# Optimization experiments

Measured on AMD Instinct MI355X. Metric: run time of the kernel, lower is better.

## Reference

```python
import jax, jax.numpy as jnp
import numpy as np

N_NODES = 100000
N_EDGES = 1600000
D_IN = 64
D_HID = 64


def setup_inputs() -> dict:
    key = jax.random.key(0)
    k1, k2, k3, k4, k5 = jax.random.split(key, 5)
    features = jax.random.normal(k1, (N_NODES, D_IN), dtype=jnp.float32)
    src = jax.random.randint(k2, (N_EDGES,), 0, N_NODES, dtype=jnp.int64)
    dst = jax.random.randint(k3, (N_EDGES,), 0, N_NODES, dtype=jnp.int64)
    # nn.Linear(in_feats, n_hidden): W is [out, in], b is [out]
    W = jax.random.normal(k4, (D_HID, D_IN), dtype=jnp.float32) * (1.0 / np.sqrt(D_IN))
    b = jax.random.normal(k5, (D_HID,), dtype=jnp.float32) * 0.01
    return {"features": features, "src": src, "dst": dst, "W": W, "b": b}


def reference(features, src, dst, W, b):
    # copy_src + sum: h_agg[v] = sum_{(u->v) in E} features[u]
    msgs = features[src]                                   # [E, D_IN] gather
    h_agg = jax.ops.segment_sum(msgs, dst, num_segments=N_NODES)  # [N, D_IN] scatter-add
    # NodeApplyModule: linear + activation
    h = h_agg @ W.T + b                                    # [N, D_HID]
    return jax.nn.relu(h)
```

## Files before the change

kernel.cpp:

```cpp
#include <hip/hip_runtime.h>
#include <hip/hip_bf16.h>

constexpr int N_NODES = 100000;
constexpr int N_EDGES = 1600000;
constexpr int D = 64;
constexpr int NPB = 64;
constexpr int NBUK = (N_NODES + NPB - 1) / NPB;
constexpr int CAP = 1536;
constexpr int CAP_E = 2304;
constexpr unsigned SENT = 100000u;
constexpr int PART_BLOCKS = 256;
constexpr int CONV_BLOCKS = 64;
constexpr int PREP_THREADS = 1024;
constexpr int EPB = (N_EDGES + PART_BLOCKS - 1) / PART_BLOCKS;

__device__ inline unsigned pack_bf16_2(float a, float b) {
    unsigned ua = __float_as_uint(a), ub = __float_as_uint(b);
    ua = (ua + 0x7FFFu + ((ua >> 16) & 1u)) >> 16;
    ub = (ub + 0x7FFFu + ((ub >> 16) & 1u)) >> 16;
    return ua | (ub << 16);
}

__global__ __launch_bounds__(PREP_THREADS) void prep_kernel(
    const float* __restrict__ feat, const int* __restrict__ src,
    const int* __restrict__ dst, int* __restrict__ gtot,
    unsigned* __restrict__ packed, uint2* __restrict__ fb) {
    const int tid = threadIdx.x;

    if (blockIdx.x >= PART_BLOCKS) {
        const int cb = blockIdx.x - PART_BLOCKS;
        const int total = N_NODES * D / 4;
        const float4* f4 = reinterpret_cast<const float4*>(feat);
        for (int i = cb * PREP_THREADS + tid; i < total; i += CONV_BLOCKS * PREP_THREADS) {
            const float4 v = f4[i];
            fb[i] = make_uint2(pack_bf16_2(v.x, v.y), pack_bf16_2(v.z, v.w));
        }
        if (cb == 0 && tid < 16)
            fb[(size_t)SENT * 16 + tid] = make_uint2(0u, 0u);
        return;
    }

    __shared__ int lcnt[NBUK];
    __shared__ int lbase[NBUK];

    const int lo = blockIdx.x * EPB;
    int hi = lo + EPB; if (hi > N_EDGES) hi = N_EDGES;

    for (int i = tid; i < NBUK; i += PREP_THREADS) lcnt[i] = 0;
    __syncthreads();

    #pragma unroll 4
    for (int e = lo + tid; e < hi; e += PREP_THREADS)
        atomicAdd(&lcnt[dst[e] >> 6], 1);
    __syncthreads();

    for (int i = tid; i < NBUK; i += PREP_THREADS) {
        const int c = lcnt[i];
        lbase[i] = c ? atomicAdd(&gtot[i], c) : 0;
        lcnt[i] = 0;
    }
    __syncthreads();

    #pragma unroll 4
    for (int e = lo + tid; e < hi; e += PREP_THREADS) {
        const int d = dst[e];
        const int buk = d >> 6;
        const int p = lbase[buk] + atomicAdd(&lcnt[buk], 1);
        if (p < CAP)
            packed[(size_t)buk * CAP + p] =
                ((unsigned)(d & (NPB - 1)) << 17) | (unsigned)src[e];
    }
}

__global__ __launch_bounds__(256, 2) void bucket_kernel(
    const uint2* __restrict__ fb, const int* __restrict__ gtot,
    const unsigned* __restrict__ packed, const float* __restrict__ W,
    const float* __restrict__ bias, float* __restrict__ out) {
    __shared__ unsigned elist[CAP_E];
    __shared__ int cnt[NPB];
    __shared__ int cur[NPB];
    __shared__ int pstart[NPB];
    __shared__ float hrow[4][D];

    const int tid = threadIdx.x;
    const int w = tid >> 6;
    const int j = tid & 63;
    const int g = j >> 4;
    const int l = j & 15;
    const int buk = blockIdx.x;

    float4 wr[16];
    #pragma unroll
    for (int q = 0; q < 16; ++q)
        wr[q] = *reinterpret_cast<const float4*>(W + j * D + (q << 2));
    const float bj = bias[j];

    int m = gtot[buk]; if (m > CAP) m = CAP;
    const unsigned* bp = packed + (size_t)buk * CAP;

    unsigned pk0 = 0, pk1 = 0, pk2 = 0, pk3 = 0, pk4 = 0, pk5 = 0;
    const bool v0 = tid < m,            v1 = tid + 256 < m;
    const bool v2 = tid + 512 < m,      v3 = tid + 768 < m;
    const bool v4 = tid + 1024 < m,     v5 = tid + 1280 < m;
    if (v0) pk0 = bp[tid];
    if (v1) pk1 = bp[tid + 256];
    if (v2) pk2 = bp[tid + 512];
    if (v3) pk3 = bp[tid + 768];
    if (v4) pk4 = bp[tid + 1024];
    if (v5) pk5 = bp[tid + 1280];

    if (tid < NPB) cnt[tid] = 0;
    for (int i = tid; i < CAP_E; i += 256) elist[i] = SENT;
    __syncthreads();

    if (v0) atomicAdd(&cnt[pk0 >> 17], 1);
    if (v1) atomicAdd(&cnt[pk1 >> 17], 1);
    if (v2) atomicAdd(&cnt[pk2 >> 17], 1);
    if (v3) atomicAdd(&cnt[pk3 >> 17], 1);
    if (v4) atomicAdd(&cnt[pk4 >> 17], 1);
    if (v5) atomicAdd(&cnt[pk5 >> 17], 1);
    __syncthreads();

    if (tid < 64) {
        const int c = cnt[tid];
        const int pc = (c + 15) & ~15;
        int x = pc;
        #pragma unroll
        for (int o = 1; o < 64; o <<= 1) {
            const int y = __shfl_up(x, o);
            if (tid >= o) x += y;
        }
        pstart[tid] = x - pc;
        cur[tid] = x - pc;
    }
    __syncthreads();

    if (v0) { const int p = atomicAdd(&cur[pk0 >> 17], 1); elist[p] = pk0 & 0x1FFFFu; }
    if (v1) { const int p = atomicAdd(&cur[pk1 >> 17], 1); elist[p] = pk1 & 0x1FFFFu; }
    if (v2) { const int p = atomicAdd(&cur[pk2 >> 17], 1); elist[p] = pk2 & 0x1FFFFu; }
    if (v3) { const int p = atomicAdd(&cur[pk3 >> 17], 1); elist[p] = pk3 & 0x1FFFFu; }
    if (v4) { const int p = atomicAdd(&cur[pk4 >> 17], 1); elist[p] = pk4 & 0x1FFFFu; }
    if (v5) { const int p = atomicAdd(&cur[pk5 >> 17], 1); elist[p] = pk5 & 0x1FFFFu; }
    __syncthreads();

    const int gbase = buk * NPB;
    const int n0 = w << 4;

    int pf = pstart[n0];
    uint2 q0 = fb[(size_t)elist[pf + g] * 16 + l];
    uint2 q1 = fb[(size_t)elist[pf + 4 + g] * 16 + l];
    uint2 q2 = fb[(size_t)elist[pf + 8 + g] * 16 + l];
    uint2 q3 = fb[(size_t)elist[pf + 12 + g] * 16 + l];

    for (int n = n0; n < n0 + 16; ++n) {
        int i = pstart[n];
        const int e1 = i + ((cnt[n] + 15) & ~15);
        const int nextstart = (n + 1 < NPB) ? pstart[n + 1] : 0;

        float hx = 0.f, hy = 0.f, hz = 0.f, hw_ = 0.f;

        while (i < e1) {
            const int i_nxt = (i + 16 < e1) ? (i + 16) : nextstart;
            const int t0 = elist[i_nxt + g];
            const int t1 = elist[i_nxt + 4 + g];
            const int t2 = elist[i_nxt + 8 + g];
            const int t3 = elist[i_nxt + 12 + g];
            const uint2 r0 = fb[(size_t)t0 * 16 + l];
            const uint2 r1 = fb[(size_t)t1 * 16 + l];
            const uint2 r2 = fb[(size_t)t2 * 16 + l];
            const uint2 r3 = fb[(size_t)t3 * 16 + l];
            hx += __uint_as_float(q0.x << 16) + __uint_as_float(q1.x << 16)
                + __uint_as_float(q2.x << 16) + __uint_as_float(q3.x << 16);
            hy += __uint_as_float(q0.x & 0xFFFF0000u) + __uint_as_float(q1.x & 0xFFFF0000u)
                + __uint_as_float(q2.x & 0xFFFF0000u) + __uint_as_float(q3.x & 0xFFFF0000u);
            hz += __uint_as_float(q0.y << 16) + __uint_as_float(q1.y << 16)
                + __uint_as_float(q2.y << 16) + __uint_as_float(q3.y << 16);
            hw_ += __uint_as_float(q0.y & 0xFFFF0000u) + __uint_as_float(q1.y & 0xFFFF0000u)
                 + __uint_as_float(q2.y & 0xFFFF0000u) + __uint_as_float(q3.y & 0xFFFF0000u);
            q0 = r0; q1 = r1; q2 = r2; q3 = r3;
            i += 16;
        }

        hx += __shfl_xor(hx, 16); hx += __shfl_xor(hx, 32);
        hy += __shfl_xor(hy, 16); hy += __shfl_xor(hy, 32);
        hz += __shfl_xor(hz, 16); hz += __shfl_xor(hz, 32);
        hw_ += __shfl_xor(hw_, 16); hw_ += __shfl_xor(hw_, 32);

        if (g == 0)
            *reinterpret_cast<float4*>(&hrow[w][l << 2]) =
                make_float4(hx, hy, hz, hw_);

        float acc = bj;
        #pragma unroll
        for (int q = 0; q < 16; ++q) {
            const float4 hv = *reinterpret_cast<const float4*>(&hrow[w][q << 2]);
            acc = fmaf(hv.x, wr[q].x, acc);
            acc = fmaf(hv.y, wr[q].y, acc);
            acc = fmaf(hv.z, wr[q].z, acc);
            acc = fmaf(hv.w, wr[q].w, acc);
        }
        const int gn = gbase + n;
        if (gn < N_NODES) out[(size_t)gn * D + j] = fmaxf(acc, 0.0f);
    }
}

extern "C" void kernel_launch(void* const* d_in, const int* in_sizes, int n_in,
                              void* d_out, int out_size, void* d_ws, size_t ws_size,
                              hipStream_t stream) {
    const float* feat = (const float*)d_in[0];
    const int*   src  = (const int*)d_in[1];
    const int*   dst  = (const int*)d_in[2];
    const float* W    = (const float*)d_in[3];
    const float* b    = (const float*)d_in[4];
    float* out = (float*)d_out;

    int* gtot = (int*)d_ws;
    unsigned* packed = (unsigned*)((char*)d_ws + 8192);
    uint2* fb = (uint2*)((char*)d_ws + 8192 + (size_t)NBUK * CAP * 4);

    hipMemsetAsync(gtot, 0, NBUK * sizeof(int), stream);

    prep_kernel<<<PART_BLOCKS + CONV_BLOCKS, PREP_THREADS, 0, stream>>>(
        feat, src, dst, gtot, packed, fb);

    bucket_kernel<<<NBUK, 256, 0, stream>>>(fb, gtot, packed, W, b, out);
}
```

Before: 102.0 us.

## Pad per-node edge lists to 8 and preload dst in partition kernel

The bucket kernel now pads each node's edge list to a multiple of 8 instead of 16, halving the in-flight gathers per step (2 instead of 4 rows prefetched). This reduces wasted sentinel gathers for nodes with around 16 edges and lets the shared edge list shrink. The prep kernel loads all dst values for its chunk up front into registers and reuses them in both the count and scatter passes instead of reloading them. The trade-off is less memory-level parallelism per wave in the gather loop.

```diff
diff --git a/kernel.cpp b/kernel.cpp
--- a/kernel.cpp
+++ b/kernel.cpp
@@ -7,7 +7,7 @@
 constexpr int NPB = 64;
 constexpr int NBUK = (N_NODES + NPB - 1) / NPB;
 constexpr int CAP = 1536;
-constexpr int CAP_E = 2304;
+constexpr int CAP_E = 2048;
 constexpr unsigned SENT = 100000u;
 constexpr int PART_BLOCKS = 256;
 constexpr int CONV_BLOCKS = 64;
@@ -43,15 +43,31 @@
     __shared__ int lcnt[NBUK];
     __shared__ int lbase[NBUK];
 
-    const int lo = blockIdx.x * EPB;
-    int hi = lo + EPB; if (hi > N_EDGES) hi = N_EDGES;
+    const int base = blockIdx.x * EPB + tid;
+
+    int d0 = 0, d1 = 0, d2 = 0, d3 = 0, d4 = 0, d5 = 0, d6 = 0;
+    const bool k0 = tid            < EPB, k1 = tid + 1024 < EPB;
+    const bool k2 = tid + 2048 < EPB,     k3 = tid + 3072 < EPB;
+    const bool k4 = tid + 4096 < EPB,     k5 = tid + 5120 < EPB;
+    const bool k6 = tid + 6144 < EPB;
+    if (k0) d0 = dst[base];
+    if (k1) d1 = dst[base + 1024];
+    if (k2) d2 = dst[base + 2048];
+    if (k3) d3 = dst[base + 3072];
+    if (k4) d4 = dst[base + 4096];
+    if (k5) d5 = dst[base + 5120];
+    if (k6) d6 = dst[base + 6144];
 
     for (int i = tid; i < NBUK; i += PREP_THREADS) lcnt[i] = 0;
     __syncthreads();
 
-    #pragma unroll 4
-    for (int e = lo + tid; e < hi; e += PREP_THREADS)
-        atomicAdd(&lcnt[dst[e] >> 6], 1);
+    if (k0) atomicAdd(&lcnt[d0 >> 6], 1);
+    if (k1) atomicAdd(&lcnt[d1 >> 6], 1);
+    if (k2) atomicAdd(&lcnt[d2 >> 6], 1);
+    if (k3) atomicAdd(&lcnt[d3 >> 6], 1);
+    if (k4) atomicAdd(&lcnt[d4 >> 6], 1);
+    if (k5) atomicAdd(&lcnt[d5 >> 6], 1);
+    if (k6) atomicAdd(&lcnt[d6 >> 6], 1);
     __syncthreads();
 
     for (int i = tid; i < NBUK; i += PREP_THREADS) {
@@ -61,15 +77,23 @@
     }
     __syncthreads();
 
-    #pragma unroll 4
-    for (int e = lo + tid; e < hi; e += PREP_THREADS) {
-        const int d = dst[e];
-        const int buk = d >> 6;
-        const int p = lbase[buk] + atomicAdd(&lcnt[buk], 1);
-        if (p < CAP)
-            packed[(size_t)buk * CAP + p] =
-                ((unsigned)(d & (NPB - 1)) << 17) | (unsigned)src[e];
-    }
+    #define SCATTER(kk, dd, off)                                              \
+        if (kk) {                                                             \
+            const int s = src[base + off];                                    \
+            const int buk = dd >> 6;                                          \
+            const int p = lbase[buk] + atomicAdd(&lcnt[buk], 1);              \
+            if (p < CAP)                                                      \
+                packed[(size_t)buk * CAP + p] =                               \
+                    ((unsigned)(dd & (NPB - 1)) << 17) | (unsigned)s;         \
+        }
+    SCATTER(k0, d0, 0)
+    SCATTER(k1, d1, 1024)
+    SCATTER(k2, d2, 2048)
+    SCATTER(k3, d3, 3072)
+    SCATTER(k4, d4, 4096)
+    SCATTER(k5, d5, 5120)
+    SCATTER(k6, d6, 6144)
+    #undef SCATTER
 }
 
 __global__ __launch_bounds__(256, 2) void bucket_kernel(
@@ -110,7 +134,8 @@
     if (v5) pk5 = bp[tid + 1280];
 
     if (tid < NPB) cnt[tid] = 0;
-    for (int i = tid; i < CAP_E; i += 256) elist[i] = SENT;
+    #pragma unroll
+    for (int i = 0; i < CAP_E / 256; ++i) elist[tid + i * 256] = SENT;
     __syncthreads();
 
     if (v0) atomicAdd(&cnt[pk0 >> 17], 1);
@@ -123,7 +148,7 @@
 
     if (tid < 64) {
         const int c = cnt[tid];
-        const int pc = (c + 15) & ~15;
+        const int pc = (c + 7) & ~7;
         int x = pc;
         #pragma unroll
         for (int o = 1; o < 64; o <<= 1) {
@@ -146,39 +171,29 @@
     const int gbase = buk * NPB;
     const int n0 = w << 4;
 
-    int pf = pstart[n0];
+    const int pf = pstart[n0];
     uint2 q0 = fb[(size_t)elist[pf + g] * 16 + l];
     uint2 q1 = fb[(size_t)elist[pf + 4 + g] * 16 + l];
-    uint2 q2 = fb[(size_t)elist[pf + 8 + g] * 16 + l];
-    uint2 q3 = fb[(size_t)elist[pf + 12 + g] * 16 + l];
 
     for (int n = n0; n < n0 + 16; ++n) {
         int i = pstart[n];
-        const int e1 = i + ((cnt[n] + 15) & ~15);
+        const int e1 = i + ((cnt[n] + 7) & ~7);
         const int nextstart = (n + 1 < NPB) ? pstart[n + 1] : 0;
 
         float hx = 0.f, hy = 0.f, hz = 0.f, hw_ = 0.f;
 
         while (i < e1) {
-            const int i_nxt = (i + 16 < e1) ? (i + 16) : nextstart;
+            const int i_nxt = (i + 8 < e1) ? (i + 8) : nextstart;
             const int t0 = elist[i_nxt + g];
             const int t1 = elist[i_nxt + 4 + g];
-            const int t2 = elist[i_nxt + 8 + g];
-            const int t3 = elist[i_nxt + 12 + g];
             const uint2 r0 = fb[(size_t)t0 * 16 + l];
             const uint2 r1 = fb[(size_t)t1 * 16 + l];
-            const uint2 r2 = fb[(size_t)t2 * 16 + l];
-            const uint2 r3 = fb[(size_t)t3 * 16 + l];
-            hx += __uint_as_float(q0.x << 16) + __uint_as_float(q1.x << 16)
-                + __uint_as_float(q2.x << 16) + __uint_as_float(q3.x << 16);
-            hy += __uint_as_float(q0.x & 0xFFFF0000u) + __uint_as_float(q1.x & 0xFFFF0000u)
-                + __uint_as_float(q2.x & 0xFFFF0000u) + __uint_as_float(q3.x & 0xFFFF0000u);
-            hz += __uint_as_float(q0.y << 16) + __uint_as_float(q1.y << 16)
-                + __uint_as_float(q2.y << 16) + __uint_as_float(q3.y << 16);
-            hw_ += __uint_as_float(q0.y & 0xFFFF0000u) + __uint_as_float(q1.y & 0xFFFF0000u)
-                 + __uint_as_float(q2.y & 0xFFFF0000u) + __uint_as_float(q3.y & 0xFFFF0000u);
-            q0 = r0; q1 = r1; q2 = r2; q3 = r3;
-            i += 16;
+            hx += __uint_as_float(q0.x << 16) + __uint_as_float(q1.x << 16);
+            hy += __uint_as_float(q0.x & 0xFFFF0000u) + __uint_as_float(q1.x & 0xFFFF0000u);
+            hz += __uint_as_float(q0.y << 16) + __uint_as_float(q1.y << 16);
+            hw_ += __uint_as_float(q0.y & 0xFFFF0000u) + __uint_as_float(q1.y & 0xFFFF0000u);
+            q0 = r0; q1 = r1;
+            i += 8;
         }
 
         hx += __shfl_xor(hx, 16); hx += __shfl_xor(hx, 32);
```

Result: faster. 98.79 us (-3.1%).
